# Kernel optimization log

Hardware: AMD Instinct MI355X
Metric: run time of the kernel (lower is better)

The kernel has to match this reference:

```python
import jax, jax.numpy as jnp
import numpy as np

B, S, E = 2, 2048, 1024
H, D = 16, 64  # num_head, num_hidden
EPS = 1e-5

def setup_inputs() -> dict:
    key = jax.random.key(0)
    ks = jax.random.split(key, 12)
    sc_e = 1.0 / np.sqrt(E)
    sc_hd = 1.0 / np.sqrt(H * D)
    return {
        "q": jax.random.normal(ks[0], (B, S, E), jnp.float32),
        "k": jax.random.normal(ks[1], (B, S, E), jnp.float32),
        "v": jax.random.normal(ks[2], (B, S, E), jnp.float32),
        "Wq": jax.random.normal(ks[3], (E, H * D), jnp.float32) * sc_e,
        "bq": jnp.zeros((H * D,), jnp.float32),
        "Wk": jax.random.normal(ks[4], (E, H * D), jnp.float32) * sc_e,
        "bk": jnp.zeros((H * D,), jnp.float32),
        "Wv": jax.random.normal(ks[5], (E, H * D), jnp.float32) * sc_e,
        "bv": jnp.zeros((H * D,), jnp.float32),
        "Wo": jax.random.normal(ks[6], (H * D, E), jnp.float32) * sc_hd,
        "bo": jnp.zeros((E,), jnp.float32),
        "gamma": jnp.ones((E,), jnp.float32),
        "beta": jnp.zeros((E,), jnp.float32),
    }

def reference(q, k, v, Wq, bq, Wk, bk, Wv, bv, Wo, bo, gamma, beta):
    # QKV projections -> [B, H, S, D]
    q_ = (q @ Wq + bq).reshape(B, S, H, D).transpose(0, 2, 1, 3)
    k_ = (k @ Wk + bk).reshape(B, S, H, D).transpose(0, 2, 1, 3)
    v_ = (v @ Wv + bv).reshape(B, S, H, D).transpose(0, 2, 1, 3)
    # scaled dot-product attention scores [B, H, Sq, Sk]
    qk = jnp.einsum('bhid,bhjd->bhij', q_, k_) / np.sqrt(D)
    attn = jax.nn.softmax(qk, axis=-1)
    # weighted values -> [B, Sq, H, D] -> [B, Sq, H*D]
    outs = jnp.einsum('bhij,bhjd->bihd', attn, v_).reshape(B, S, H * D)
    outs = outs @ Wo + bo
    # residual + LayerNorm
    x = outs + q
    mu = jnp.mean(x, axis=-1, keepdims=True)
    var = jnp.var(x, axis=-1, keepdims=True)
    y = (x - mu) * jax.lax.rsqrt(var + EPS) * gamma + beta
    return (y, attn)
```

## Files before the change

kernel.cpp:

```cpp
#include <hip/hip_runtime.h>

typedef unsigned short u16;
typedef __attribute__((ext_vector_type(8))) short bf16x8;
typedef __attribute__((ext_vector_type(4))) float f32x4;
typedef __attribute__((ext_vector_type(4))) unsigned short u16x4;

static __device__ __forceinline__ u16 f2bf(float f) {
  unsigned int u = __builtin_bit_cast(unsigned int, f);
  u += 0x7fffu + ((u >> 16) & 1u);
  return (u16)(u >> 16);
}

static __device__ __forceinline__ void load_lds16(const void* g, void* l) {
  __builtin_amdgcn_global_load_lds(
      (const __attribute__((address_space(1))) void*)g,
      (__attribute__((address_space(3))) void*)l,
      16, 0, 0);
}

__global__ __launch_bounds__(256) void to_bf16_3(const float* __restrict__ a,
                                                 const float* __restrict__ b,
                                                 const float* __restrict__ c,
                                                 u16* __restrict__ oa,
                                                 u16* __restrict__ ob,
                                                 u16* __restrict__ oc, int n4) {
  const int z = blockIdx.y;
  const float* in = (z == 0) ? a : (z == 1) ? b : c;
  u16* out = (z == 0) ? oa : (z == 1) ? ob : oc;
  int i = blockIdx.x * 256 + threadIdx.x;
  if (i < n4) {
    float4 f = ((const float4*)in)[i];
    u16x4 u;
    u[0] = f2bf(f.x); u[1] = f2bf(f.y); u[2] = f2bf(f.z); u[3] = f2bf(f.w);
    ((u16x4*)out)[i] = u;
  }
}

__global__ __launch_bounds__(256) void transpose_bf16_4(
    const float* __restrict__ Wq, const float* __restrict__ Wk,
    const float* __restrict__ Wv, const float* __restrict__ Wo,
    u16* __restrict__ WqT, u16* __restrict__ WkT,
    u16* __restrict__ WvT, u16* __restrict__ WoT) {
  const int z = blockIdx.z;
  const float* W = (z == 0) ? Wq : (z == 1) ? Wk : (z == 2) ? Wv : Wo;
  u16* WT = (z == 0) ? WqT : (z == 1) ? WkT : (z == 2) ? WvT : WoT;
  __shared__ float t[32][33];
  const int tx = threadIdx.x & 31, ty = threadIdx.x >> 5;
  const int bx = blockIdx.x * 32, by = blockIdx.y * 32;
#pragma unroll
  for (int r = ty; r < 32; r += 8) t[r][tx] = W[(size_t)(by + r) * 1024 + bx + tx];
  __syncthreads();
#pragma unroll
  for (int r = ty; r < 32; r += 8) WT[(size_t)(bx + r) * 1024 + by + tx] = f2bf(t[tx][r]);
}

__device__ __forceinline__ void gemm_core(const u16* __restrict__ A,
                                          const u16* __restrict__ BT,
                                          int m0, int n0,
                                          u16* As, u16* Bs, f32x4 acc[4][4]) {
  const int tid = threadIdx.x;
  const int w = tid >> 6, l = tid & 63;
  const int lr = l & 15, lg = l >> 4;
  const int wm = w >> 1, wn = w & 1;

  const int p0 = tid * 16, p1 = p0 + 4096;
  const char* gA0 = (const char*)A + (size_t)(m0 + (p0 >> 6)) * 2048 + (p0 & 63);
  const char* gA1 = (const char*)A + (size_t)(m0 + (p1 >> 6)) * 2048 + (p1 & 63);
  const char* gB0 = (const char*)BT + (size_t)(n0 + (p0 >> 6)) * 2048 + (p0 & 63);
  const char* gB1 = (const char*)BT + (size_t)(n0 + (p1 >> 6)) * 2048 + (p1 & 63);

#define GCSTAGE(bb, kb)                                                      \
  load_lds16(gA0 + (kb), (char*)As + (bb) * 8192 + w * 1024);                \
  load_lds16(gA1 + (kb), (char*)As + (bb) * 8192 + 4096 + w * 1024);         \
  load_lds16(gB0 + (kb), (char*)Bs + (bb) * 8192 + w * 1024);                \
  load_lds16(gB1 + (kb), (char*)Bs + (bb) * 8192 + 4096 + w * 1024);

  GCSTAGE(0, 0);
  __syncthreads();
  for (int kt = 0; kt < 32; ++kt) {
    const int bb = kt & 1;
    if (kt < 31) { GCSTAGE(bb ^ 1, (kt + 1) * 64); }
    const u16* as = As + bb * 4096;
    const u16* bs = Bs + bb * 4096;
    bf16x8 av[4], bv[4];
#pragma unroll
    for (int f = 0; f < 4; ++f) {
      av[f] = *(const bf16x8*)(as + (wm * 64 + f * 16 + lr) * 32 + lg * 8);
      bv[f] = *(const bf16x8*)(bs + (wn * 64 + f * 16 + lr) * 32 + lg * 8);
    }
#pragma unroll
    for (int fm = 0; fm < 4; ++fm)
#pragma unroll
      for (int fn = 0; fn < 4; ++fn)
        acc[fm][fn] = __builtin_amdgcn_mfma_f32_16x16x32_bf16(av[fm], bv[fn],
                                                              acc[fm][fn], 0, 0, 0);
    asm volatile("s_waitcnt vmcnt(0)" ::: "memory");
    __builtin_amdgcn_sched_barrier(0);
    __builtin_amdgcn_s_barrier();
  }
#undef GCSTAGE
}

__global__ __launch_bounds__(256) void qkv_gemm(
    const u16* __restrict__ qb, const u16* __restrict__ kbm, const u16* __restrict__ vbm,
    const u16* __restrict__ WqT, const u16* __restrict__ WkT, const u16* __restrict__ WvT,
    const float* __restrict__ bq, const float* __restrict__ bk, const float* __restrict__ bv,
    u16* __restrict__ Qb, u16* __restrict__ Kb, u16* __restrict__ Vt) {
  __shared__ u16 As[2 * 4096], Bs[2 * 4096];
  const int z = blockIdx.z;
  const u16* A = (z == 0) ? qb : (z == 1) ? kbm : vbm;
  const u16* BT = (z == 0) ? WqT : (z == 1) ? WkT : WvT;
  const float* bias = (z == 0) ? bq : (z == 1) ? bk : bv;
  const int m0 = blockIdx.x * 128, n0 = blockIdx.y * 128;

  f32x4 acc[4][4];
#pragma unroll
  for (int i = 0; i < 4; ++i)
#pragma unroll
    for (int j = 0; j < 4; ++j) acc[i][j] = (f32x4){0.f, 0.f, 0.f, 0.f};

  gemm_core(A, BT, m0, n0, As, Bs, acc);

  const int tid = threadIdx.x;
  const int w = tid >> 6, l = tid & 63, lr = l & 15, lg = l >> 4;
  const int wm = w >> 1, wn = w & 1;
#pragma unroll
  for (int fm = 0; fm < 4; ++fm)
#pragma unroll
    for (int fn = 0; fn < 4; ++fn)
#pragma unroll
      for (int r = 0; r < 4; ++r) {
        const int m = m0 + wm * 64 + fm * 16 + lg * 4 + r;
        const int n = n0 + wn * 64 + fn * 16 + lr;
        const float val = acc[fm][fn][r] + bias[n];
        const int b = m >> 11, s = m & 2047, hh = n >> 6, d = n & 63;
        const u16 u = f2bf(val);
        if (z == 2)
          Vt[(((size_t)b * 16 + hh) * 64 + d) * 2048 + s] = u;
        else if (z == 0)
          Qb[(((size_t)b * 16 + hh) * 2048 + s) * 64 + d] = u;
        else
          Kb[(((size_t)b * 16 + hh) * 2048 + s) * 64 + d] = u;
      }
}

__global__ __launch_bounds__(256) void o_gemm(
    const u16* __restrict__ Ao, const u16* __restrict__ WoT,
    const float* __restrict__ bo, const float* __restrict__ resid,
    float* __restrict__ x) {
  __shared__ u16 As[2 * 4096], Bs[2 * 4096];
  const int m0 = blockIdx.x * 128, n0 = blockIdx.y * 128;
  f32x4 acc[4][4];
#pragma unroll
  for (int i = 0; i < 4; ++i)
#pragma unroll
    for (int j = 0; j < 4; ++j) acc[i][j] = (f32x4){0.f, 0.f, 0.f, 0.f};

  gemm_core(Ao, WoT, m0, n0, As, Bs, acc);

  const int tid = threadIdx.x;
  const int w = tid >> 6, l = tid & 63, lr = l & 15, lg = l >> 4;
  const int wm = w >> 1, wn = w & 1;
#pragma unroll
  for (int fm = 0; fm < 4; ++fm)
#pragma unroll
    for (int fn = 0; fn < 4; ++fn)
#pragma unroll
      for (int r = 0; r < 4; ++r) {
        const int m = m0 + wm * 64 + fm * 16 + lg * 4 + r;
        const int n = n0 + wn * 64 + fn * 16 + lr;
        const size_t idx = (size_t)m * 1024 + n;
        x[idx] = acc[fm][fn][r] + bo[n] + resid[idx];
      }
}

__global__ __launch_bounds__(256, 4) void denom_kernel(
    const u16* __restrict__ Qb, const u16* __restrict__ Kb,
    float* __restrict__ Ld) {
  __shared__ u16 Kbuf[2][4096];
  const int tid = threadIdx.x;
  const int w = tid >> 6, l = tid & 63, lr = l & 15, lg = l >> 4;

  int flat = blockIdx.x;
  flat = (flat & 7) * 64 + (flat >> 3);
  const int it = flat & 15, bh = flat >> 4;
  const int i0 = it * 128;

  const char* KhB = (const char*)(Kb + (size_t)bh * 2048 * 64);
  const u16* Q0 = Qb + ((size_t)bh * 2048 + i0 + w * 32 + lr) * 64;
  const bf16x8 q00 = *(const bf16x8*)(Q0 + lg * 8);
  const bf16x8 q01 = *(const bf16x8*)(Q0 + 32 + lg * 8);
  const bf16x8 q10 = *(const bf16x8*)(Q0 + 16 * 64 + lg * 8);
  const bf16x8 q11 = *(const bf16x8*)(Q0 + 16 * 64 + 32 + lg * 8);

  const int srow = l >> 3;
  const int soff = ((l & 7) ^ srow) << 4;
  const int rsw = (lr & 7) << 4;

#define STAGE_K(bb, j0)                                                      \
  load_lds16(KhB + (size_t)((j0) + w * 8 + srow) * 128 + soff,               \
             (char*)Kbuf[bb] + w * 1024);                                    \
  load_lds16(KhB + (size_t)((j0) + 32 + w * 8 + srow) * 128 + soff,          \
             (char*)Kbuf[bb] + w * 1024 + 4096);

  f32x4 ls0 = (f32x4){0.f, 0.f, 0.f, 0.f}, ls1 = ls0;
  STAGE_K(0, 0);
  __syncthreads();
  for (int jt = 0; jt < 32; ++jt) {
    const int bb = jt & 1;
    if (jt < 31) { STAGE_K(bb ^ 1, (jt + 1) * 64); }
    const char* kb = (const char*)Kbuf[bb];
#pragma unroll
    for (int t = 0; t < 4; ++t) {
      const bf16x8 k0 = *(const bf16x8*)(kb + (t * 16 + lr) * 128 + ((lg * 16) ^ rsw));
      const bf16x8 k1 = *(const bf16x8*)(kb + (t * 16 + lr) * 128 + ((64 + lg * 16) ^ rsw));
      f32x4 c0 = (f32x4){0.f, 0.f, 0.f, 0.f}, c1 = c0;
      c0 = __builtin_amdgcn_mfma_f32_16x16x32_bf16(k0, q00, c0, 0, 0, 0);
      c0 = __builtin_amdgcn_mfma_f32_16x16x32_bf16(k1, q01, c0, 0, 0, 0);
      c1 = __builtin_amdgcn_mfma_f32_16x16x32_bf16(k0, q10, c1, 0, 0, 0);
      c1 = __builtin_amdgcn_mfma_f32_16x16x32_bf16(k1, q11, c1, 0, 0, 0);
      ls0[0] += __expf(c0[0] * 0.125f);
      ls0[1] += __expf(c0[1] * 0.125f);
      ls0[2] += __expf(c0[2] * 0.125f);
      ls0[3] += __expf(c0[3] * 0.125f);
      ls1[0] += __expf(c1[0] * 0.125f);
      ls1[1] += __expf(c1[1] * 0.125f);
      ls1[2] += __expf(c1[2] * 0.125f);
      ls1[3] += __expf(c1[3] * 0.125f);
    }
    __syncthreads();
  }
#undef STAGE_K
  float s0 = ls0[0] + ls0[1] + ls0[2] + ls0[3];
  s0 += __shfl_xor(s0, 16);
  s0 += __shfl_xor(s0, 32);
  float s1 = ls1[0] + ls1[1] + ls1[2] + ls1[3];
  s1 += __shfl_xor(s1, 16);
  s1 += __shfl_xor(s1, 32);
  if (l < 16) {
    Ld[(size_t)bh * 2048 + i0 + w * 32 + l] = s0;
    Ld[(size_t)bh * 2048 + i0 + w * 32 + 16 + l] = s1;
  }
}

__global__ __launch_bounds__(256, 4) void attn3_kernel(
    const u16* __restrict__ Qb, const u16* __restrict__ Kb,
    const u16* __restrict__ Vt, const float* __restrict__ Ld,
    float* __restrict__ attnG, u16* __restrict__ outattn) {
  __shared__ u16 Kbuf[2][4096];
  __shared__ u16 Vbuf[2][4096];
  __shared__ u16 Pbuf[4][1024];
  const int tid = threadIdx.x;
  const int w = tid >> 6, l = tid & 63, lr = l & 15, lg = l >> 4;

  int flat = (blockIdx.z * 16 + blockIdx.y) * 32 + blockIdx.x;
  flat = (flat & 7) * 128 + (flat >> 3);
  const int qt = flat & 31, h = (flat >> 5) & 15, b = flat >> 9;
  const int bh = b * 16 + h;
  const int i0 = qt * 64 + w * 16;

  const char* KhB = (const char*)(Kb + (size_t)bh * 2048 * 64);
  const char* VhB = (const char*)(Vt + (size_t)bh * 64 * 2048);
  const u16* Qrow = Qb + ((size_t)bh * 2048 + i0 + lr) * 64;
  const bf16x8 bq0 = *(const bf16x8*)(Qrow + lg * 8);
  const bf16x8 bq1 = *(const bf16x8*)(Qrow + 32 + lg * 8);
  const float inv = 1.f / Ld[(size_t)bh * 2048 + i0 + lr];

  const int srow = l >> 3;
  const int soff = ((l & 7) ^ srow) << 4;
  const int rsw = (lr & 7) << 4;

#define STAGE_K(bb, j0)                                                      \
  load_lds16(KhB + (size_t)((j0) + w * 8 + srow) * 128 + soff,               \
             (char*)Kbuf[bb] + w * 1024);                                    \
  load_lds16(KhB + (size_t)((j0) + 32 + w * 8 + srow) * 128 + soff,          \
             (char*)Kbuf[bb] + w * 1024 + 4096);
#define STAGE_V(bb, j0)                                                      \
  load_lds16(VhB + (size_t)(w * 8 + srow) * 4096 + (size_t)(j0) * 2 + soff,  \
             (char*)Vbuf[bb] + w * 1024);                                    \
  load_lds16(VhB + (size_t)(32 + w * 8 + srow) * 4096 + (size_t)(j0) * 2 +   \
                 soff,                                                       \
             (char*)Vbuf[bb] + w * 1024 + 4096);

  float* const awb = attnG + ((size_t)bh * 2048 + i0 + (l >> 4)) * 2048 + (l & 15) * 4;
  char* const Pw = (char*)Pbuf[w];
  f32x4 o0 = (f32x4){0.f, 0.f, 0.f, 0.f}, o1 = o0, o2 = o0, o3 = o0;

  STAGE_K(0, 0);
  STAGE_V(0, 0);
  __syncthreads();
  for (int jt = 0; jt < 32; ++jt) {
    const int bb = jt & 1;
    if (jt < 31) {
      STAGE_K(bb ^ 1, (jt + 1) * 64);
      STAGE_V(bb ^ 1, (jt + 1) * 64);
    }
    const char* kb = (const char*)Kbuf[bb];
    const char* vb = (const char*)Vbuf[bb];
    const int j0 = jt * 64;
#pragma unroll
    for (int t = 0; t < 4; ++t) {
      const bf16x8 k0 = *(const bf16x8*)(kb + (t * 16 + lr) * 128 + ((lg * 16) ^ rsw));
      const bf16x8 k1 = *(const bf16x8*)(kb + (t * 16 + lr) * 128 + ((64 + lg * 16) ^ rsw));
      f32x4 c = (f32x4){0.f, 0.f, 0.f, 0.f};
      c = __builtin_amdgcn_mfma_f32_16x16x32_bf16(k0, bq0, c, 0, 0, 0);
      c = __builtin_amdgcn_mfma_f32_16x16x32_bf16(k1, bq1, c, 0, 0, 0);
      u16x4 pu;
      pu[0] = f2bf(__expf(c[0] * 0.125f) * inv);
      pu[1] = f2bf(__expf(c[1] * 0.125f) * inv);
      pu[2] = f2bf(__expf(c[2] * 0.125f) * inv);
      pu[3] = f2bf(__expf(c[3] * 0.125f) * inv);
      *(u16x4*)(Pw + lr * 128 + ((t * 32 + lg * 8) ^ rsw)) = pu;
    }
#pragma unroll
    for (int rq = 0; rq < 4; ++rq) {
      const int row = rq * 4 + (l >> 4);
      const u16x4 pb = *(const u16x4*)(Pw + row * 128 +
                                       (((l & 15) * 8) ^ ((row & 7) << 4)));
      f32x4 pf;
      pf[0] = __builtin_bit_cast(float, (unsigned)(unsigned short)pb[0] << 16);
      pf[1] = __builtin_bit_cast(float, (unsigned)(unsigned short)pb[1] << 16);
      pf[2] = __builtin_bit_cast(float, (unsigned)(unsigned short)pb[2] << 16);
      pf[3] = __builtin_bit_cast(float, (unsigned)(unsigned short)pb[3] << 16);
      __builtin_nontemporal_store(pf, (f32x4*)(awb + (size_t)(rq * 4) * 2048 + j0));
    }
#pragma unroll
    for (int half = 0; half < 2; ++half) {
      const int jjb = half * 64;
      const bf16x8 pa = *(const bf16x8*)(Pw + lr * 128 + ((jjb + lg * 16) ^ rsw));
      const bf16x8 v0 = *(const bf16x8*)(vb + (0 * 16 + lr) * 128 + ((jjb + lg * 16) ^ rsw));
      const bf16x8 v1 = *(const bf16x8*)(vb + (1 * 16 + lr) * 128 + ((jjb + lg * 16) ^ rsw));
      const bf16x8 v2 = *(const bf16x8*)(vb + (2 * 16 + lr) * 128 + ((jjb + lg * 16) ^ rsw));
      const bf16x8 v3 = *(const bf16x8*)(vb + (3 * 16 + lr) * 128 + ((jjb + lg * 16) ^ rsw));
      o0 = __builtin_amdgcn_mfma_f32_16x16x32_bf16(pa, v0, o0, 0, 0, 0);
      o1 = __builtin_amdgcn_mfma_f32_16x16x32_bf16(pa, v1, o1, 0, 0, 0);
      o2 = __builtin_amdgcn_mfma_f32_16x16x32_bf16(pa, v2, o2, 0, 0, 0);
      o3 = __builtin_amdgcn_mfma_f32_16x16x32_bf16(pa, v3, o3, 0, 0, 0);
    }
    asm volatile("s_waitcnt vmcnt(4)" ::: "memory");
    __builtin_amdgcn_sched_barrier(0);
    __builtin_amdgcn_s_barrier();
  }
#undef STAGE_K
#undef STAGE_V

#pragma unroll
  for (int r = 0; r < 4; ++r) {
    u16* orow = outattn + ((size_t)b * 2048 + i0 + lg * 4 + r) * 1024 + h * 64 + lr;
    orow[0]  = f2bf(o0[r]);
    orow[16] = f2bf(o1[r]);
    orow[32] = f2bf(o2[r]);
    orow[48] = f2bf(o3[r]);
  }
}

__global__ __launch_bounds__(256) void ln_kernel(const float* __restrict__ x,
                                                 const float* __restrict__ gamma,
                                                 const float* __restrict__ beta,
                                                 float* __restrict__ y) {
  const int row = blockIdx.x, t = threadIdx.x;
  const float4 xv = *(const float4*)(x + (size_t)row * 1024 + t * 4);
  float s = xv.x + xv.y + xv.z + xv.w;
  float q2 = xv.x * xv.x + xv.y * xv.y + xv.z * xv.z + xv.w * xv.w;
#pragma unroll
  for (int off = 32; off >= 1; off >>= 1) {
    s += __shfl_xor(s, off);
    q2 += __shfl_xor(q2, off);
  }
  __shared__ float ps[4], pq[4];
  const int w = t >> 6, l = t & 63;
  if (l == 0) { ps[w] = s; pq[w] = q2; }
  __syncthreads();
  s = ps[0] + ps[1] + ps[2] + ps[3];
  q2 = pq[0] + pq[1] + pq[2] + pq[3];
  const float mu = s * (1.f / 1024.f);
  const float var = q2 * (1.f / 1024.f) - mu * mu;
  const float rs = rsqrtf(var + 1e-5f);
  const float4 g = *(const float4*)(gamma + t * 4);
  const float4 bb = *(const float4*)(beta + t * 4);
  float4 o;
  o.x = (xv.x - mu) * rs * g.x + bb.x;
  o.y = (xv.y - mu) * rs * g.y + bb.y;
  o.z = (xv.z - mu) * rs * g.z + bb.z;
  o.w = (xv.w - mu) * rs * g.w + bb.w;
  *(float4*)(y + (size_t)row * 1024 + t * 4) = o;
}

extern "C" void kernel_launch(void* const* d_in, const int* in_sizes, int n_in,
                              void* d_out, int out_size, void* d_ws, size_t ws_size,
                              hipStream_t stream) {
  (void)in_sizes; (void)n_in; (void)out_size; (void)ws_size;
  const float* q = (const float*)d_in[0];
  const float* k = (const float*)d_in[1];
  const float* v = (const float*)d_in[2];
  const float* Wq = (const float*)d_in[3];
  const float* bq = (const float*)d_in[4];
  const float* Wk = (const float*)d_in[5];
  const float* bk = (const float*)d_in[6];
  const float* Wv = (const float*)d_in[7];
  const float* bv = (const float*)d_in[8];
  const float* Wo = (const float*)d_in[9];
  const float* bo = (const float*)d_in[10];
  const float* gamma = (const float*)d_in[11];
  const float* beta = (const float*)d_in[12];

  char* ws = (char*)d_ws;
  const size_t MB = 1ull << 20;
  u16* WqT = (u16*)(ws + 0 * MB);
  u16* WkT = (u16*)(ws + 2 * MB);
  u16* WvT = (u16*)(ws + 4 * MB);
  u16* WoT = (u16*)(ws + 6 * MB);
  u16* qb  = (u16*)(ws + 8 * MB);
  float* Ld = (float*)(ws + 10 * MB);
  u16* kb  = (u16*)(ws + 16 * MB);
  u16* vb  = (u16*)(ws + 24 * MB);
  u16* Qb  = (u16*)(ws + 32 * MB);
  u16* Kb  = (u16*)(ws + 40 * MB);
  u16* Vt  = (u16*)(ws + 48 * MB);
  u16* oa  = (u16*)(ws + 56 * MB);
  float* x = (float*)(ws + 64 * MB);

  float* y = (float*)d_out;
  float* attnG = y + 4194304;

  to_bf16_3<<<dim3(4096, 3), 256, 0, stream>>>(q, k, v, qb, kb, vb, 1048576);
  transpose_bf16_4<<<dim3(32, 32, 4), 256, 0, stream>>>(Wq, Wk, Wv, Wo,
                                                        WqT, WkT, WvT, WoT);
  qkv_gemm<<<dim3(32, 8, 3), 256, 0, stream>>>(qb, kb, vb, WqT, WkT, WvT,
                                               bq, bk, bv, Qb, Kb, Vt);
  denom_kernel<<<512, 256, 0, stream>>>(Qb, Kb, Ld);
  attn3_kernel<<<dim3(32, 16, 2), 256, 0, stream>>>(Qb, Kb, Vt, Ld, attnG, oa);
  o_gemm<<<dim3(32, 8), 256, 0, stream>>>(oa, WoT, bo, q, x);
  ln_kernel<<<4096, 256, 0, stream>>>(x, gamma, beta, y);
}
```

Before: 258.9 us.

## Merge prep kernels, halve o_gemm M tile, raise priority during PV MFMAs

The bf16 conversion and weight-transpose kernels become a single launch, which removes one kernel launch and its gap. The output-projection GEMM now uses 64-row tiles, giving 512 blocks instead of 256 so more of the 256 CUs are kept busy, at the cost of less reuse per block. The attention kernel raises wave priority around the P·V MFMA section so those waves get issue preference over waves doing exp and stores. These are three unrelated changes touching different stages.

```diff
diff --git a/kernel.cpp b/kernel.cpp
--- a/kernel.cpp
+++ b/kernel.cpp
@@ -18,35 +18,32 @@
       16, 0, 0);
 }
 
-__global__ __launch_bounds__(256) void to_bf16_3(const float* __restrict__ a,
-                                                 const float* __restrict__ b,
-                                                 const float* __restrict__ c,
-                                                 u16* __restrict__ oa,
-                                                 u16* __restrict__ ob,
-                                                 u16* __restrict__ oc, int n4) {
+__global__ __launch_bounds__(256) void prep_kernel(
+    const float* __restrict__ q, const float* __restrict__ k,
+    const float* __restrict__ v,
+    u16* __restrict__ qb, u16* __restrict__ kb, u16* __restrict__ vb,
+    const float* __restrict__ Wq, const float* __restrict__ Wk,
+    const float* __restrict__ Wv, const float* __restrict__ Wo,
+    u16* __restrict__ WqT, u16* __restrict__ WkT,
+    u16* __restrict__ WvT, u16* __restrict__ WoT) {
   const int z = blockIdx.y;
-  const float* in = (z == 0) ? a : (z == 1) ? b : c;
-  u16* out = (z == 0) ? oa : (z == 1) ? ob : oc;
-  int i = blockIdx.x * 256 + threadIdx.x;
-  if (i < n4) {
+  if (z < 3) {
+    const float* in = (z == 0) ? q : (z == 1) ? k : v;
+    u16* out = (z == 0) ? qb : (z == 1) ? kb : vb;
+    const int i = blockIdx.x * 256 + threadIdx.x;
     float4 f = ((const float4*)in)[i];
     u16x4 u;
     u[0] = f2bf(f.x); u[1] = f2bf(f.y); u[2] = f2bf(f.z); u[3] = f2bf(f.w);
     ((u16x4*)out)[i] = u;
-  }
-}
-
-__global__ __launch_bounds__(256) void transpose_bf16_4(
-    const float* __restrict__ Wq, const float* __restrict__ Wk,
-    const float* __restrict__ Wv, const float* __restrict__ Wo,
-    u16* __restrict__ WqT, u16* __restrict__ WkT,
-    u16* __restrict__ WvT, u16* __restrict__ WoT) {
-  const int z = blockIdx.z;
-  const float* W = (z == 0) ? Wq : (z == 1) ? Wk : (z == 2) ? Wv : Wo;
-  u16* WT = (z == 0) ? WqT : (z == 1) ? WkT : (z == 2) ? WvT : WoT;
+    return;
+  }
+  const int bid = blockIdx.x;
+  const int wt = bid >> 10, tile = bid & 1023;
+  const float* W = (wt == 0) ? Wq : (wt == 1) ? Wk : (wt == 2) ? Wv : Wo;
+  u16* WT = (wt == 0) ? WqT : (wt == 1) ? WkT : (wt == 2) ? WvT : WoT;
   __shared__ float t[32][33];
   const int tx = threadIdx.x & 31, ty = threadIdx.x >> 5;
-  const int bx = blockIdx.x * 32, by = blockIdx.y * 32;
+  const int bx = (tile & 31) * 32, by = (tile >> 5) * 32;
 #pragma unroll
   for (int r = ty; r < 32; r += 8) t[r][tx] = W[(size_t)(by + r) * 1024 + bx + tx];
   __syncthreads();
@@ -99,6 +96,53 @@
     __builtin_amdgcn_s_barrier();
   }
 #undef GCSTAGE
+}
+
+__device__ __forceinline__ void gemm_core64(const u16* __restrict__ A,
+                                            const u16* __restrict__ BT,
+                                            int m0, int n0,
+                                            u16* As, u16* Bs, f32x4 acc[2][4]) {
+  const int tid = threadIdx.x;
+  const int w = tid >> 6, l = tid & 63;
+  const int lr = l & 15, lg = l >> 4;
+  const int wm = w >> 1, wn = w & 1;
+
+  const int pA = tid * 16;
+  const int pB0 = tid * 16, pB1 = pB0 + 4096;
+  const char* gA = (const char*)A + (size_t)(m0 + (pA >> 6)) * 2048 + (pA & 63);
+  const char* gB0 = (const char*)BT + (size_t)(n0 + (pB0 >> 6)) * 2048 + (pB0 & 63);
+  const char* gB1 = (const char*)BT + (size_t)(n0 + (pB1 >> 6)) * 2048 + (pB1 & 63);
+
+#define GC64STAGE(bb, kb)                                                    \
+  load_lds16(gA + (kb), (char*)As + (bb) * 4096 + w * 1024);                 \
+  load_lds16(gB0 + (kb), (char*)Bs + (bb) * 8192 + w * 1024);                \
+  load_lds16(gB1 + (kb), (char*)Bs + (bb) * 8192 + 4096 + w * 1024);
+
+  GC64STAGE(0, 0);
+  __syncthreads();
+  for (int kt = 0; kt < 32; ++kt) {
+    const int bb = kt & 1;
+    if (kt < 31) { GC64STAGE(bb ^ 1, (kt + 1) * 64); }
+    const u16* as = As + bb * 2048;
+    const u16* bs = Bs + bb * 4096;
+    bf16x8 av[2], bv[4];
+#pragma unroll
+    for (int f = 0; f < 2; ++f)
+      av[f] = *(const bf16x8*)(as + (wm * 32 + f * 16 + lr) * 32 + lg * 8);
+#pragma unroll
+    for (int f = 0; f < 4; ++f)
+      bv[f] = *(const bf16x8*)(bs + (wn * 64 + f * 16 + lr) * 32 + lg * 8);
+#pragma unroll
+    for (int fm = 0; fm < 2; ++fm)
+#pragma unroll
+      for (int fn = 0; fn < 4; ++fn)
+        acc[fm][fn] = __builtin_amdgcn_mfma_f32_16x16x32_bf16(av[fm], bv[fn],
+                                                              acc[fm][fn], 0, 0, 0);
+    asm volatile("s_waitcnt vmcnt(0)" ::: "memory");
+    __builtin_amdgcn_sched_barrier(0);
+    __builtin_amdgcn_s_barrier();
+  }
+#undef GC64STAGE
 }
 
 __global__ __launch_bounds__(256) void qkv_gemm(
@@ -148,26 +192,26 @@
     const u16* __restrict__ Ao, const u16* __restrict__ WoT,
     const float* __restrict__ bo, const float* __restrict__ resid,
     float* __restrict__ x) {
-  __shared__ u16 As[2 * 4096], Bs[2 * 4096];
-  const int m0 = blockIdx.x * 128, n0 = blockIdx.y * 128;
-  f32x4 acc[4][4];
-#pragma unroll
-  for (int i = 0; i < 4; ++i)
+  __shared__ u16 As[2 * 2048], Bs[2 * 4096];
+  const int m0 = blockIdx.x * 64, n0 = blockIdx.y * 128;
+  f32x4 acc[2][4];
+#pragma unroll
+  for (int i = 0; i < 2; ++i)
 #pragma unroll
     for (int j = 0; j < 4; ++j) acc[i][j] = (f32x4){0.f, 0.f, 0.f, 0.f};
 
-  gemm_core(Ao, WoT, m0, n0, As, Bs, acc);
+  gemm_core64(Ao, WoT, m0, n0, As, Bs, acc);
 
   const int tid = threadIdx.x;
   const int w = tid >> 6, l = tid & 63, lr = l & 15, lg = l >> 4;
   const int wm = w >> 1, wn = w & 1;
 #pragma unroll
-  for (int fm = 0; fm < 4; ++fm)
+  for (int fm = 0; fm < 2; ++fm)
 #pragma unroll
     for (int fn = 0; fn < 4; ++fn)
 #pragma unroll
       for (int r = 0; r < 4; ++r) {
-        const int m = m0 + wm * 64 + fm * 16 + lg * 4 + r;
+        const int m = m0 + wm * 32 + fm * 16 + lg * 4 + r;
         const int n = n0 + wn * 64 + fn * 16 + lr;
         const size_t idx = (size_t)m * 1024 + n;
         x[idx] = acc[fm][fn][r] + bo[n] + resid[idx];
@@ -324,6 +368,7 @@
       pf[3] = __builtin_bit_cast(float, (unsigned)(unsigned short)pb[3] << 16);
       __builtin_nontemporal_store(pf, (f32x4*)(awb + (size_t)(rq * 4) * 2048 + j0));
     }
+    __builtin_amdgcn_s_setprio(1);
 #pragma unroll
     for (int half = 0; half < 2; ++half) {
       const int jjb = half * 64;
@@ -337,6 +382,7 @@
       o2 = __builtin_amdgcn_mfma_f32_16x16x32_bf16(pa, v2, o2, 0, 0, 0);
       o3 = __builtin_amdgcn_mfma_f32_16x16x32_bf16(pa, v3, o3, 0, 0, 0);
     }
+    __builtin_amdgcn_s_setprio(0);
     asm volatile("s_waitcnt vmcnt(4)" ::: "memory");
     __builtin_amdgcn_sched_barrier(0);
     __builtin_amdgcn_s_barrier();
@@ -423,13 +469,13 @@
   float* y = (float*)d_out;
   float* attnG = y + 4194304;
 
-  to_bf16_3<<<dim3(4096, 3), 256, 0, stream>>>(q, k, v, qb, kb, vb, 1048576);
-  transpose_bf16_4<<<dim3(32, 32, 4), 256, 0, stream>>>(Wq, Wk, Wv, Wo,
-                                                        WqT, WkT, WvT, WoT);
+  prep_kernel<<<dim3(4096, 4), 256, 0, stream>>>(q, k, v, qb, kb, vb,
+                                                 Wq, Wk, Wv, Wo,
+                                                 WqT, WkT, WvT, WoT);
   qkv_gemm<<<dim3(32, 8, 3), 256, 0, stream>>>(qb, kb, vb, WqT, WkT, WvT,
                                                bq, bk, bv, Qb, Kb, Vt);
   denom_kernel<<<512, 256, 0, stream>>>(Qb, Kb, Ld);
   attn3_kernel<<<dim3(32, 16, 2), 256, 0, stream>>>(Qb, Kb, Vt, Ld, attnG, oa);
-  o_gemm<<<dim3(32, 8), 256, 0, stream>>>(oa, WoT, bo, q, x);
+  o_gemm<<<dim3(64, 8), 256, 0, stream>>>(oa, WoT, bo, q, x);
   ln_kernel<<<4096, 256, 0, stream>>>(x, gamma, beta, y);
 }
```

Result: faster. 253.1 us (-2.2%).
